# Optimization experiments

Hardware: AMD Instinct MI355X
Metric: run time of the kernel (lower is better)

The kernel has to match this reference:

```python
import jax, jax.numpy as jnp
import numpy as np

N, E = 10000, 160000          # nodes, edges
MUL = 128                     # channel multiplicity of 0e and 1o blocks
NSP = 10                      # node_attrs (species one-hot) dim
NRAD = 8                      # edge_feats radial basis dim
SILU_C = 1.6790               # e3nn normalize2mom constant for SiLU
AVG_NEIGH = 16.0
SQ3 = np.sqrt(3.0).astype(np.float32)


def setup_inputs() -> dict:
    key = jax.random.key(0)
    ks = jax.random.split(key, 14)
    d = {}
    d["node_feats"] = jax.random.normal(ks[0], (N, 4 * MUL), jnp.float32)   # [N, 128 + 128*3]
    d["node_attrs"] = jax.random.normal(ks[1], (N, NSP), jnp.float32)
    d["edge_feats"] = jax.random.normal(ks[2], (E, NRAD), jnp.float32)
    d["edge_attrs"] = jax.random.normal(ks[3], (E, 4), jnp.float32)          # [0e | 1o]
    d["edge_index"] = jax.random.randint(ks[4], (2, E), 0, N, jnp.int32)
    # e3nn internal weights are standard normal; normalization applied in forward
    d["lin1_ws"] = jax.random.normal(ks[5], (MUL, MUL), jnp.float32)
    d["lin1_wv"] = jax.random.normal(ks[6], (MUL, MUL), jnp.float32)
    d["fc_w0"] = jax.random.normal(ks[7], (NRAD, 64), jnp.float32)
    d["fc_w1"] = jax.random.normal(ks[8], (64, 64), jnp.float32)
    d["fc_w2"] = jax.random.normal(ks[9], (64, 4 * MUL), jnp.float32)        # tp.weight_numel = 512
    d["lin2_ws"] = jax.random.normal(ks[10], (2 * MUL, MUL), jnp.float32)    # 256x0e -> 128x0e
    d["lin2_wv"] = jax.random.normal(ks[11], (2 * MUL, MUL), jnp.float32)    # 256x1o -> 128x1o
    d["sc_ws"] = jax.random.normal(ks[12], (MUL, NSP, MUL), jnp.float32)
    d["sc_wv"] = jax.random.normal(ks[13], (MUL, NSP, MUL), jnp.float32)
    return d


def _fc(ef, w0, w1, w2):
    # e3nn FullyConnectedNet: x @ W / sqrt(fan_in), normalize2mom-scaled SiLU between layers
    h = SILU_C * jax.nn.silu(ef @ w0 / np.float32(np.sqrt(NRAD)))
    h = SILU_C * jax.nn.silu(h @ w1 / np.float32(8.0))
    return h @ w2 / np.float32(8.0)


def reference(node_feats, node_attrs, edge_feats, edge_attrs, edge_index,
              lin1_ws, lin1_wv, fc_w0, fc_w1, fc_w2,
              lin2_ws, lin2_wv, sc_ws, sc_wv):
    x_s = node_feats[:, :MUL]                       # [N, 128] scalar block
    x_v = node_feats[:, MUL:].reshape(N, MUL, 3)    # [N, 128, 3] vector block

    # self-connection: FullyConnectedTensorProduct with 10x0e attrs; path weight 1/sqrt(mul1*mul2)
    sc_norm = np.float32(1.0 / np.sqrt(MUL * NSP))
    sc_s = jnp.einsum('nu,nv,uvw->nw', x_s, node_attrs, sc_ws) * sc_norm
    sc_v = jnp.einsum('nuc,nv,uvw->nwc', x_v, node_attrs, sc_wv) * sc_norm

    # linear_1 (per-irrep channel mixing, fan_in = 128)
    l1 = np.float32(1.0 / np.sqrt(MUL))
    y_s = (x_s @ lin1_ws) * l1
    y_v = jnp.einsum('nuc,uw->nwc', x_v, lin1_wv) * l1

    src = edge_index[1]
    dst = edge_index[0]
    xs_e = y_s[src]                                 # [E, 128]
    xv_e = y_v[src]                                 # [E, 128, 3]
    a_s = edge_attrs[:, :1]                         # [E, 1]
    a_v = edge_attrs[:, 1:]                         # [E, 3]

    w = _fc(edge_feats, fc_w0, fc_w1, fc_w2)        # [E, 512]
    w_ss, w_sv, w_vs, w_vv = jnp.split(w, 4, axis=1)  # instruction order in source

    # 'uvu' weighted tensor product with e3nn component/element normalization:
    # net coefficient per path works out to 1 except 1o x 1o -> 0e which is 1/sqrt(3)
    mid_s0 = w_ss * xs_e * a_s                                          # 0e*0e->0e
    mid_s1 = w_vv * jnp.einsum('euc,ec->eu', xv_e, a_v) / SQ3           # 1o*1o->0e
    mid_v2 = (w_sv * xs_e)[:, :, None] * a_v[:, None, :]                # 0e*1o->1o
    mid_v3 = w_vs[:, :, None] * xv_e * a_s[:, :, None]                  # 1o*0e->1o

    inv = np.float32(1.0 / np.sqrt(AVG_NEIGH))
    s = jax.ops.segment_sum(jnp.concatenate([mid_s0, mid_s1], axis=1), dst, num_segments=N) * inv  # [N, 256]
    v = jax.ops.segment_sum(jnp.concatenate([mid_v2, mid_v3], axis=1), dst, num_segments=N) * inv  # [N, 256, 3]

    # linear_2 (fan_in = 256)
    l2 = np.float32(1.0 / np.sqrt(2 * MUL))
    out_s = (s @ lin2_ws) * l2 + sc_s
    out_v = jnp.einsum('nuc,uw->nwc', v, lin2_wv) * l2 + sc_v

    return jnp.concatenate([out_s, out_v.reshape(N, 3 * MUL)], axis=1)   # [N, 512]
```

## Files before the change

### kernel.cpp

```cpp
#include <hip/hip_runtime.h>
#include <hip/hip_bf16.h>
#include <math.h>

#define N_NODES 10000
#define N_EDGES 160000
#define SO_BLK 157
#define VO_BLK 469

typedef __attribute__((ext_vector_type(8))) short short8x;
typedef __attribute__((ext_vector_type(4))) float floatx4;
typedef __attribute__((ext_vector_type(4))) unsigned int uint4x;
typedef __attribute__((ext_vector_type(2))) unsigned int uint2x;

union S8 { short8x v; unsigned short u[8]; uint4 q; };
union U2 { uint2x v; unsigned short us[4]; };

__device__ __forceinline__ unsigned short f2bf(float x) {
    unsigned int u = __float_as_uint(x);
    return (unsigned short)((u + 0x7fffu + ((u >> 16) & 1u)) >> 16);
}
__device__ __forceinline__ float bf2f(unsigned short u) {
    return __uint_as_float(((unsigned)u) << 16);
}
__device__ __forceinline__ float silu_c(float x) {
    return 1.679f * x / (1.0f + __expf(-x));
}

__global__ __launch_bounds__(256) void pack_all_kernel(
    const float* __restrict__ sc_ws, const float* __restrict__ lin2_ws,
    const float* __restrict__ sc_wv, const float* __restrict__ lin2_wv,
    const float* __restrict__ fc_w2, const float* __restrict__ fc_w1,
    const float* __restrict__ lin1_ws, const float* __restrict__ lin1_wv,
    unsigned short* __restrict__ b_pre, unsigned short* __restrict__ w2a,
    unsigned short* __restrict__ w1a, unsigned short* __restrict__ b_lin)
{
    const int bid = blockIdx.x;
    const int t = threadIdx.x;
    if (bid < 192) {
        int id = bid * 256 + t;
        int mat = id / 24576;
        int slot = id - mat * 24576;
        int ks = slot >> 9;
        int rr = slot & 511;
        int lane = rr & 63;
        int quad = lane >> 4;
        int n = ((rr >> 6) << 4) + (lane & 15);
        const float* sc  = mat ? sc_wv  : sc_ws;
        const float* lin = mat ? lin2_wv : lin2_ws;
        S8 pk;
        #pragma unroll
        for (int j = 0; j < 8; j++) {
            int k = ks * 32 + quad * 8 + j;
            float w;
            if (k < 1280) {
                int u = k & 127, v = k >> 7;
                w = sc[(u * 10 + v) * 128 + n];
            } else {
                w = lin[(k - 1280) * 128 + n];
            }
            pk.u[j] = f2bf(w);
        }
        *(uint4*)(b_pre + (size_t)id * 8) = pk.q;
    } else if (bid < 208) {
        int id = (bid - 192) * 256 + t;
        int lane = id & 63;
        int mfg = (id >> 6) & 31;
        int ks = id >> 11;
        int col = mfg * 16 + (lane & 15);
        int k0 = ks * 32 + (lane >> 4) * 8;
        S8 pk;
        #pragma unroll
        for (int j = 0; j < 8; j++)
            pk.u[j] = f2bf(fc_w2[(k0 + j) * 512 + col] * 0.125f);
        *(uint4*)(w2a + (size_t)id * 8) = pk.q;
    } else if (bid < 210) {
        int id = (bid - 208) * 256 + t;
        int lane = id & 63;
        int mf = (id >> 6) & 3;
        int ks = id >> 8;
        int m = mf * 16 + (lane & 15);
        int k0 = ks * 32 + (lane >> 4) * 8;
        S8 pk;
        #pragma unroll
        for (int j = 0; j < 8; j++)
            pk.u[j] = f2bf(fc_w1[(k0 + j) * 64 + m] * 0.125f);
        *(uint4*)(w1a + (size_t)id * 8) = pk.q;
    } else {
        int id = (bid - 210) * 256 + t;
        int mat = id >> 11;
        int slot = id & 2047;
        int ks = slot >> 9;
        int rr = slot & 511;
        int nf = rr >> 6;
        int lane = rr & 63;
        int n = nf * 16 + (lane & 15);
        int k0 = ks * 32 + (lane >> 4) * 8;
        const float* w = mat ? lin1_wv : lin1_ws;
        const float l1 = 0.0883883476483f;
        S8 pk;
        #pragma unroll
        for (int j = 0; j < 8; j++)
            pk.u[j] = f2bf(w[(k0 + j) * 128 + n] * l1);
        *(uint4*)(b_lin + (size_t)id * 8) = pk.q;
    }
}

__global__ __launch_bounds__(256) void node_lin1_mfma(
    const float* __restrict__ node_feats,
    const unsigned short* __restrict__ b_lin,
    unsigned short* __restrict__ y_pk,
    unsigned short* __restrict__ xvP16)
{
    __shared__ __align__(16) unsigned char smem[32768];
    short8x* Al = (short8x*)smem;
    unsigned short* Yt = (unsigned short*)smem;

    const int blk = blockIdx.x;
    const int t = threadIdx.x;
    const int base = blk * 32;
    const int lane = t & 63;
    const int wv = t >> 6;
    const int m15 = lane & 15;
    const int k0q = (lane >> 4) * 8;

    #pragma unroll
    for (int it = 0; it < 8; it++) {
        int g = wv * 8 + it;
        int af = g >> 2;
        int ks = g & 3;
        int m = af * 16 + m15;
        int comp = m >> 5;
        int nloc = m & 31;
        int node = base + nloc;
        int valid = (node < N_NODES);
        if (!valid) node = N_NODES - 1;
        int k0 = ks * 32 + k0q;
        const float* row = node_feats + (size_t)node * 512;
        S8 pk;
        if (comp == 0) {
            float4 a = *(const float4*)&row[k0];
            float4 b = *(const float4*)&row[k0 + 4];
            pk.u[0] = f2bf(a.x); pk.u[1] = f2bf(a.y); pk.u[2] = f2bf(a.z); pk.u[3] = f2bf(a.w);
            pk.u[4] = f2bf(b.x); pk.u[5] = f2bf(b.y); pk.u[6] = f2bf(b.z); pk.u[7] = f2bf(b.w);
        } else {
            int c = comp - 1;
            #pragma unroll
            for (int j = 0; j < 8; j++)
                pk.u[j] = f2bf(row[128 + (k0 + j) * 3 + c]);
            if (valid)
                *(uint4*)&xvP16[((size_t)node * 3 + c) * 128 + k0] = pk.q;
        }
        Al[(ks * 8 + af) * 64 + lane] = pk.v;
    }
    __syncthreads();

    floatx4 c[8][2];
    #pragma unroll
    for (int af = 0; af < 8; af++) {
        c[af][0] = (floatx4){0.f, 0.f, 0.f, 0.f};
        c[af][1] = (floatx4){0.f, 0.f, 0.f, 0.f};
    }

    const uint4* bq = (const uint4*)b_lin;
    #pragma unroll
    for (int ks = 0; ks < 4; ks++) {
        S8 bs0, bs1, bv0, bv1;
        bs0.q = bq[       ks*512 + (wv*2+0)*64 + lane];
        bs1.q = bq[       ks*512 + (wv*2+1)*64 + lane];
        bv0.q = bq[2048 + ks*512 + (wv*2+0)*64 + lane];
        bv1.q = bq[2048 + ks*512 + (wv*2+1)*64 + lane];
        #pragma unroll
        for (int af = 0; af < 8; af++) {
            short8x a = Al[(ks*8 + af)*64 + lane];
            if (af < 2) {
                c[af][0] = __builtin_amdgcn_mfma_f32_16x16x32_bf16(a, bs0.v, c[af][0], 0, 0, 0);
                c[af][1] = __builtin_amdgcn_mfma_f32_16x16x32_bf16(a, bs1.v, c[af][1], 0, 0, 0);
            } else {
                c[af][0] = __builtin_amdgcn_mfma_f32_16x16x32_bf16(a, bv0.v, c[af][0], 0, 0, 0);
                c[af][1] = __builtin_amdgcn_mfma_f32_16x16x32_bf16(a, bv1.v, c[af][1], 0, 0, 0);
            }
        }
    }
    __syncthreads();

    {
        const int rq = (lane >> 4) * 4;
        #pragma unroll
        for (int af = 0; af < 8; af++) {
            #pragma unroll
            for (int nf = 0; nf < 2; nf++) {
                int u = wv * 32 + nf * 16 + m15;
                #pragma unroll
                for (int i = 0; i < 4; i++) {
                    int m = af * 16 + rq + i;
                    int comp = m >> 5, nloc = m & 31;
                    Yt[(nloc * 128 + u) * 4 + comp] = f2bf(c[af][nf][i]);
                }
            }
        }
    }
    __syncthreads();
    {
        unsigned short* dst = y_pk + (size_t)base * 512;
        int nrem = N_NODES - base;
        #pragma unroll
        for (int it = 0; it < 8; it++) {
            int idx = it * 256 + t;
            if ((idx >> 6) < nrem)
                *(uint4*)(dst + (size_t)idx * 8) = *(const uint4*)&Yt[idx * 8];
        }
    }
}

__global__ __launch_bounds__(256) void hist_kernel(const int* __restrict__ edge_index,
                                                   int* __restrict__ deg) {
    int e = blockIdx.x * 256 + threadIdx.x;
    if (e < N_EDGES) atomicAdd(&deg[edge_index[e]], 1);
}

__global__ __launch_bounds__(1024) void scan_kernel(const int* __restrict__ deg,
                                                    int* __restrict__ row_start,
                                                    int* __restrict__ cursor) {
    __shared__ int wsum[16];
    __shared__ int carry_s;
    const int t = threadIdx.x;
    const int lane = t & 63, w = t >> 6;
    if (t == 0) carry_s = 0;
    __syncthreads();
    for (int chunk = 0; chunk < 10; chunk++) {
        int idx = chunk * 1024 + t;
        int v = (idx < N_NODES) ? deg[idx] : 0;
        int x = v;
        #pragma unroll
        for (int off = 1; off < 64; off <<= 1) {
            int yv = __shfl_up(x, off, 64);
            if (lane >= off) x += yv;
        }
        if (lane == 63) wsum[w] = x;
        __syncthreads();
        int wpre = 0;
        for (int i = 0; i < w; i++) wpre += wsum[i];
        int incl = x + wpre + carry_s;
        int excl = incl - v;
        if (idx < N_NODES) { row_start[idx] = excl; cursor[idx] = excl; }
        __syncthreads();
        if (t == 1023) carry_s = incl;
        __syncthreads();
    }
    if (t == 0) row_start[N_NODES] = carry_s;
}

__global__ __launch_bounds__(256) void scatter_kernel(const int* __restrict__ edge_index,
                                                      const float* __restrict__ edge_attrs,
                                                      int* __restrict__ cursor,
                                                      int* __restrict__ edge_list,
                                                      int* __restrict__ srcs,
                                                      float* __restrict__ ea_sorted) {
    int e = blockIdx.x * 256 + threadIdx.x;
    if (e < N_EDGES) {
        int pos = atomicAdd(&cursor[edge_index[e]], 1);
        edge_list[pos] = e;
        srcs[pos] = edge_index[N_EDGES + e];
        float4 ea = *(const float4*)(edge_attrs + (size_t)e * 4);
        *(float4*)(ea_sorted + (size_t)pos * 4) = ea;
    }
}

__global__ __launch_bounds__(256) void edge_w_mfma(
    const float* __restrict__ edge_feats,
    const int* __restrict__ edge_list,
    const float* __restrict__ fc_w0,
    const unsigned short* __restrict__ w1a,
    const unsigned short* __restrict__ w2a,
    unsigned short* __restrict__ w_pk)
{
    __shared__ __align__(16) unsigned char smem[26368];
    float* ef = (float*)smem;
    unsigned short* h0b = (unsigned short*)(smem + 2304);
    unsigned short* T   = (unsigned short*)smem;
    unsigned short* h1b = (unsigned short*)(smem + 16896);
    int* eids = (int*)(smem + 26112);

    const int blk = blockIdx.x;
    const int t = threadIdx.x;
    const int eb0 = blk * 64;
    const int lane = t & 63;
    const int wv = t >> 6;
    const int quad = lane >> 4;
    const int m15 = lane & 15;

    if (t < 64) eids[t] = edge_list[eb0 + t];
    __syncthreads();

    #pragma unroll
    for (int r = 0; r < 2; r++) {
        int idx = r * 256 + t;
        int el = idx >> 3;
        int k = idx & 7;
        ef[el * 9 + k] = edge_feats[(size_t)eids[el] * 8 + k];
    }
    __syncthreads();

    {
        const int e_loc = t >> 2;
        const int c0 = (t & 3) * 16;
        float a0[16];
        #pragma unroll
        for (int i = 0; i < 16; i++) a0[i] = 0.f;
        const float* efr = &ef[e_loc * 9];
        #pragma unroll
        for (int k = 0; k < 8; k++) {
            float ek = efr[k];
            float w[16];
            #pragma unroll
            for (int q4 = 0; q4 < 4; q4++)
                *(float4*)&w[q4*4] = *(const float4*)&fc_w0[k*64 + c0 + q4*4];
            #pragma unroll
            for (int i = 0; i < 16; i++) a0[i] += ek * w[i];
        }
        const float is8 = 0.35355339059f;
        S8 p0, p1;
        #pragma unroll
        for (int i = 0; i < 8; i++) {
            p0.u[i] = f2bf(silu_c(a0[i] * is8));
            p1.u[i] = f2bf(silu_c(a0[8 + i] * is8));
        }
        *(uint4*)&h0b[e_loc * 72 + c0]     = p0.q;
        *(uint4*)&h0b[e_loc * 72 + c0 + 8] = p1.q;
    }
    __syncthreads();

    {
        floatx4 c2[4];
        #pragma unroll
        for (int ee = 0; ee < 4; ee++) c2[ee] = (floatx4){0.f, 0.f, 0.f, 0.f};
        const uint4* w1aq = (const uint4*)w1a;
        #pragma unroll
        for (int ks = 0; ks < 2; ks++) {
            S8 afr;
            afr.q = w1aq[(ks*4 + wv)*64 + lane];
            #pragma unroll
            for (int ee = 0; ee < 4; ee++) {
                S8 bfr;
                bfr.q = *(const uint4*)&h0b[(ee*16 + m15) * 72 + ks*32 + quad*8];
                c2[ee] = __builtin_amdgcn_mfma_f32_16x16x32_bf16(afr.v, bfr.v, c2[ee], 0, 0, 0);
            }
        }
        #pragma unroll
        for (int ee = 0; ee < 4; ee++) {
            ushort4 pk = make_ushort4(f2bf(silu_c(c2[ee][0])), f2bf(silu_c(c2[ee][1])),
                                      f2bf(silu_c(c2[ee][2])), f2bf(silu_c(c2[ee][3])));
            *(ushort4*)&h1b[(ee*16 + m15) * 72 + wv*16 + quad*4] = pk;
        }
    }
    __syncthreads();

    const uint4* w2aq = (const uint4*)w2a;
    #pragma unroll 1
    for (int p = 0; p < 4; p++) {
        floatx4 c3[2][4];
        #pragma unroll
        for (int mf = 0; mf < 2; mf++)
            #pragma unroll
            for (int ee = 0; ee < 4; ee++)
                c3[mf][ee] = (floatx4){0.f, 0.f, 0.f, 0.f};

        #pragma unroll
        for (int ks = 0; ks < 2; ks++) {
            S8 bfr[4];
            #pragma unroll
            for (int ee = 0; ee < 4; ee++)
                bfr[ee].q = *(const uint4*)&h1b[(ee*16 + m15) * 72 + ks*32 + quad*8];
            #pragma unroll
            for (int mf = 0; mf < 2; mf++) {
                S8 afr;
                afr.q = w2aq[(size_t)(ks*32 + wv*8 + p*2 + mf) * 64 + lane];
                #pragma unroll
                for (int ee = 0; ee < 4; ee++)
                    c3[mf][ee] = __builtin_amdgcn_mfma_f32_16x16x32_bf16(afr.v, bfr[ee].v, c3[mf][ee], 0, 0, 0);
            }
        }

        __syncthreads();
        #pragma unroll
        for (int mf = 0; mf < 2; mf++) {
            #pragma unroll
            for (int ee = 0; ee < 4; ee++) {
                int e = ee*16 + m15;
                #pragma unroll
                for (int i = 0; i < 4; i++) {
                    int colp = mf*16 + quad*4 + i;
                    T[e*132 + colp*4 + wv] = f2bf(c3[mf][ee][i]);
                }
            }
        }
        __syncthreads();

        #pragma unroll
        for (int it = 0; it < 8; it++) {
            int idx = it * 256 + t;
            int e  = idx >> 5;
            int cu = idx & 31;
            uint2x v = *(const uint2x*)&T[e*132 + cu*4];
            unsigned short* dstp = w_pk + ((size_t)(eb0 + e) * 128 + p*32 + cu) * 4;
            __builtin_nontemporal_store(v, (uint2x*)dstp);
        }
    }
}

__global__ __launch_bounds__(256) void gather_kernel(
    const int* __restrict__ row_start,
    const int* __restrict__ srcs,
    const float* __restrict__ ea_sorted,
    const unsigned short* __restrict__ w_pk,
    const unsigned short* __restrict__ y_pk,
    float* __restrict__ accS,
    float* __restrict__ accV)
{
    __shared__ float sm[2][128][9];
    const int t = threadIdx.x;
    const int h = t >> 7;
    const int u = t & 127;
    const int n = blockIdx.x;
    const int sbeg = row_start[n];
    const int send = row_start[n + 1];

    float aS0 = 0.f, aS1 = 0.f;
    float aV2x = 0.f, aV2y = 0.f, aV2z = 0.f;
    float aV3x = 0.f, aV3y = 0.f, aV3z = 0.f;

    if (sbeg < send) {
        const int last = send - 1;
        const int i0 = sbeg + h;

        int j0 = (i0     < send) ? i0     : last;
        int j1 = (i0 + 2 < send) ? i0 + 2 : last;
        int s0 = srcs[j0];
        int s1 = srcs[j1];

        U2 wqA, wqB; ushort4 yqA, yqB; float4 eaA, eaB;
        wqA.v = __builtin_nontemporal_load((const uint2x*)(w_pk + ((size_t)j0 * 128 + u) * 4));
        eaA   = *(const float4*)(ea_sorted + (size_t)j0 * 4);
        yqA   = *(const ushort4*)(y_pk + ((size_t)s0 * 128 + u) * 4);
        wqB.v = __builtin_nontemporal_load((const uint2x*)(w_pk + ((size_t)j1 * 128 + u) * 4));
        eaB   = *(const float4*)(ea_sorted + (size_t)j1 * 4);
        yqB   = *(const ushort4*)(y_pk + ((size_t)s1 * 128 + u) * 4);

        int sP0 = srcs[(i0 + 4 < send) ? i0 + 4 : last];
        int sP1 = srcs[(i0 + 6 < send) ? i0 + 6 : last];

        for (int i = i0; i < send; i += 4) {
            {
                float wss = bf2f(wqA.us[0]), wsv = bf2f(wqA.us[1]);
                float wvs = bf2f(wqA.us[2]), wvv = bf2f(wqA.us[3]);
                float qs = bf2f(yqA.x), q0 = bf2f(yqA.y), q1 = bf2f(yqA.z), q2 = bf2f(yqA.w);
                aS0 += wss * qs * eaA.x;
                aS1 += wvv * (q0*eaA.y + q1*eaA.z + q2*eaA.w);
                float tsv = wsv * qs;
                aV2x += tsv * eaA.y; aV2y += tsv * eaA.z; aV2z += tsv * eaA.w;
                float tvs = wvs * eaA.x;
                aV3x += tvs * q0; aV3y += tvs * q1; aV3z += tvs * q2;
            }
            {
                int jn = (i + 4 < send) ? i + 4 : last;
                wqA.v = __builtin_nontemporal_load((const uint2x*)(w_pk + ((size_t)jn * 128 + u) * 4));
                eaA   = *(const float4*)(ea_sorted + (size_t)jn * 4);
                yqA   = *(const ushort4*)(y_pk + ((size_t)sP0 * 128 + u) * 4);
                sP0 = srcs[(i + 8 < send) ? i + 8 : last];
            }
            {
                float m = (i + 2 < send) ? 1.f : 0.f;
                float ex = eaB.x * m, ey = eaB.y * m, ez = eaB.z * m, ew = eaB.w * m;
                float wss = bf2f(wqB.us[0]), wsv = bf2f(wqB.us[1]);
                float wvs = bf2f(wqB.us[2]), wvv = bf2f(wqB.us[3]);
                float qs = bf2f(yqB.x), q0 = bf2f(yqB.y), q1 = bf2f(yqB.z), q2 = bf2f(yqB.w);
                aS0 += wss * qs * ex;
                aS1 += wvv * (q0*ey + q1*ez + q2*ew);
                float tsv = wsv * qs;
                aV2x += tsv * ey; aV2y += tsv * ez; aV2z += tsv * ew;
                float tvs = wvs * ex;
                aV3x += tvs * q0; aV3y += tvs * q1; aV3z += tvs * q2;
            }
            {
                int jn = (i + 6 < send) ? i + 6 : last;
                wqB.v = __builtin_nontemporal_load((const uint2x*)(w_pk + ((size_t)jn * 128 + u) * 4));
                eaB   = *(const float4*)(ea_sorted + (size_t)jn * 4);
                yqB   = *(const ushort4*)(y_pk + ((size_t)sP1 * 128 + u) * 4);
                sP1 = srcs[(i + 10 < send) ? i + 10 : last];
            }
        }
    }

    sm[h][u][0] = aS0;  sm[h][u][1] = aS1;
    sm[h][u][2] = aV2x; sm[h][u][3] = aV2y;
    sm[h][u][4] = aV2z; sm[h][u][5] = aV3x;
    sm[h][u][6] = aV3y; sm[h][u][7] = aV3z;
    __syncthreads();

    const float inv = 0.25f;
    const float s1c = 0.57735026919f * 0.25f;
    if (h == 0) {
        float v0 = sm[0][u][0] + sm[1][u][0];
        float v1 = sm[0][u][1] + sm[1][u][1];
        float v2 = sm[0][u][2] + sm[1][u][2];
        float v3 = sm[0][u][3] + sm[1][u][3];
        accS[(size_t)n * 256 + u]       = v0 * inv;
        accS[(size_t)n * 256 + 128 + u] = v1 * s1c;
        accV[((size_t)n * 3 + 0) * 256 + u] = v2 * inv;
        accV[((size_t)n * 3 + 1) * 256 + u] = v3 * inv;
    } else {
        float v4 = sm[0][u][4] + sm[1][u][4];
        float v5 = sm[0][u][5] + sm[1][u][5];
        float v6 = sm[0][u][6] + sm[1][u][6];
        float v7 = sm[0][u][7] + sm[1][u][7];
        accV[((size_t)n * 3 + 2) * 256 + u]       = v4 * inv;
        accV[((size_t)n * 3 + 0) * 256 + 128 + u] = v5 * inv;
        accV[((size_t)n * 3 + 1) * 256 + 128 + u] = v6 * inv;
        accV[((size_t)n * 3 + 2) * 256 + 128 + u] = v7 * inv;
    }
}

__global__ __launch_bounds__(256) void node_out_mfma(
    const float* __restrict__ node_feats,
    const float* __restrict__ node_attrs,
    const unsigned short* __restrict__ xvP16,
    const float* __restrict__ accS,
    const float* __restrict__ accV,
    const unsigned short* __restrict__ b_pre,
    float* __restrict__ out)
{
    __shared__ __align__(16) short8x Abuf[2][256];
    const int bid = blockIdx.x;
    const int t = threadIdx.x;
    const int lane = t & 63;
    const int wv = t >> 6;
    const bool is_s = (bid < SO_BLK);

    const int r    = ((t >> 6) << 4) + (t & 15);
    const int q8   = ((t >> 4) & 3) * 8;

    const float* px = nullptr;
    const unsigned short* pxv = nullptr;
    const float* pa;
    const float* pat;
    if (is_s) {
        int R = bid * 64 + r;
        int node = (R < N_NODES) ? R : 0;
        px  = node_feats + (size_t)node * 512;
        pa  = accS + (size_t)node * 256;
        pat = node_attrs + node * 10;
    } else {
        int Rg = (bid - SO_BLK) * 64 + r;
        if (Rg >= 3 * N_NODES) Rg = 0;
        int node = Rg / 3;
        pxv = xvP16 + (size_t)Rg * 128;
        pa  = accV + (size_t)Rg * 256;
        pat = node_attrs + node * 10;
    }

    const uint4* bb = (const uint4*)(b_pre) + (is_s ? 0 : 24576);
    const float sc_norm = 0.02795084972f;
    const float l2 = 0.0625f;

    float xf[4][8];
    S8    xh[4];
    if (is_s) {
        #pragma unroll
        for (int c = 0; c < 4; c++) {
            floatx4 lo = *(const floatx4*)&px[c*32 + q8];
            floatx4 hi = *(const floatx4*)&px[c*32 + q8 + 4];
            #pragma unroll
            for (int i = 0; i < 4; i++) { xf[c][i] = lo[i]; xf[c][4+i] = hi[i]; }
        }
    } else {
        #pragma unroll
        for (int c = 0; c < 4; c++)
            xh[c].q = *(const uint4*)&pxv[c*32 + q8];
    }
    float attC = pat[0] * sc_norm;

    floatx4 acc[4][2];
    #pragma unroll
    for (int af = 0; af < 4; af++) {
        acc[af][0] = (floatx4){0.f, 0.f, 0.f, 0.f};
        acc[af][1] = (floatx4){0.f, 0.f, 0.f, 0.f};
    }

    const int cof0 = (wv*2+0)*64 + lane;
    const int cof1 = (wv*2+1)*64 + lane;

    auto packx = [&](int c_, float att_) -> short8x {
        S8 pk;
        if (is_s) {
            #pragma unroll
            for (int i = 0; i < 8; i++) pk.u[i] = f2bf(xf[c_][i] * att_);
        } else {
            #pragma unroll
            for (int i = 0; i < 8; i++) pk.u[i] = f2bf(bf2f(xh[c_].u[i]) * att_);
        }
        return pk.v;
    };
    auto mstep = [&](int kb, const S8& b0, const S8& b1) {
        __builtin_amdgcn_s_setprio(1);
        #pragma unroll
        for (int af = 0; af < 4; af++) {
            short8x a = Abuf[kb][af*64 + lane];
            acc[af][0] = __builtin_amdgcn_mfma_f32_16x16x32_bf16(a, b0.v, acc[af][0], 0, 0, 0);
            acc[af][1] = __builtin_amdgcn_mfma_f32_16x16x32_bf16(a, b1.v, acc[af][1], 0, 0, 0);
        }
        __builtin_amdgcn_s_setprio(0);
    };
    auto bload = [&](int k2, S8& b0, S8& b1) {
        b0.q = bb[(size_t)k2*512 + cof0];
        b1.q = bb[(size_t)k2*512 + cof1];
    };
    auto barrier_ = [&]() {
        asm volatile("s_waitcnt lgkmcnt(0)" ::: "memory");
        __builtin_amdgcn_s_barrier();
    };

    S8 bA0, bA1, bB0, bB1;
    bload(0, bA0, bA1);
    bload(1, bB0, bB1);

    Abuf[0][t] = packx(0, attC);
    barrier_();

    #pragma unroll 1
    for (int vb = 0; vb < 9; vb++) {
        float attN = pat[vb + 1] * sc_norm;
        const int ksb = vb * 4;
        Abuf[1][t] = packx(1, attC); mstep(0, bA0, bA1); bload(ksb+2, bA0, bA1); barrier_();
        Abuf[0][t] = packx(2, attC); mstep(1, bB0, bB1); bload(ksb+3, bB0, bB1); barrier_();
        Abuf[1][t] = packx(3, attC); mstep(0, bA0, bA1); bload(ksb+4, bA0, bA1); barrier_();
        Abuf[0][t] = packx(0, attN); mstep(1, bB0, bB1); bload(ksb+5, bB0, bB1); barrier_();
        attC = attN;
    }

    floatx4 aT0[2], aT1[2];
    auto issue0 = [&](int k_) { int j2 = (k_-40)*32 + q8;
        aT0[0] = *(const floatx4*)&pa[j2]; aT0[1] = *(const floatx4*)&pa[j2+4]; };
    auto issue1 = [&](int k_) { int j2 = (k_-40)*32 + q8;
        aT1[0] = *(const floatx4*)&pa[j2]; aT1[1] = *(const floatx4*)&pa[j2+4]; };
    auto packT = [&](const floatx4* a2) -> short8x {
        S8 pk;
        #pragma unroll
        for (int i = 0; i < 4; i++) { pk.u[i] = f2bf(a2[0][i] * l2); pk.u[4+i] = f2bf(a2[1][i] * l2); }
        return pk.v;
    };

    Abuf[1][t] = packx(1, attC); mstep(0, bA0, bA1); bload(38, bA0, bA1); barrier_();
    Abuf[0][t] = packx(2, attC); mstep(1, bB0, bB1); bload(39, bB0, bB1); barrier_();
    issue0(40);
    Abuf[1][t] = packx(3, attC); mstep(0, bA0, bA1); bload(40, bA0, bA1); barrier_();
    issue1(41);
    Abuf[0][t] = packT(aT0); mstep(1, bB0, bB1); bload(41, bB0, bB1); barrier_();
    issue0(42);
    Abuf[1][t] = packT(aT1); mstep(0, bA0, bA1); bload(42, bA0, bA1); barrier_();
    issue1(43);
    Abuf[0][t] = packT(aT0); mstep(1, bB0, bB1); bload(43, bB0, bB1); barrier_();
    issue0(44);
    Abuf[1][t] = packT(aT1); mstep(0, bA0, bA1); bload(44, bA0, bA1); barrier_();
    issue1(45);
    Abuf[0][t] = packT(aT0); mstep(1, bB0, bB1); bload(45, bB0, bB1); barrier_();
    issue0(46);
    Abuf[1][t] = packT(aT1); mstep(0, bA0, bA1); bload(46, bA0, bA1); barrier_();
    issue1(47);
    Abuf[0][t] = packT(aT0); mstep(1, bB0, bB1); bload(47, bB0, bB1); barrier_();
    Abuf[1][t] = packT(aT1); mstep(0, bA0, bA1); barrier_();
    mstep(1, bB0, bB1);

    const int m = lane & 15;
    const int rq = (lane >> 4) * 4;
    if (is_s) {
        const int n0 = bid * 64;
        #pragma unroll
        for (int af = 0; af < 4; af++) {
            #pragma unroll
            for (int i = 0; i < 4; i++) {
                int n = n0 + af*16 + rq + i;
                if (n < N_NODES) {
                    out[(size_t)n*512 + wv*32 + m]      = acc[af][0][i];
                    out[(size_t)n*512 + wv*32 + 16 + m] = acc[af][1][i];
                }
            }
        }
    } else {
        const int r0 = (bid - SO_BLK) * 64;
        #pragma unroll
        for (int af = 0; af < 4; af++) {
            #pragma unroll
            for (int i = 0; i < 4; i++) {
                int Rg = r0 + af*16 + rq + i;
                if (Rg < 3 * N_NODES) {
                    int nn = Rg / 3;
                    int cc = Rg - nn * 3;
                    float* po = out + (size_t)nn*512 + 128 + cc;
                    po[(wv*32 + m)*3]      = acc[af][0][i];
                    po[(wv*32 + 16 + m)*3] = acc[af][1][i];
                }
            }
        }
    }
}

extern "C" void kernel_launch(void* const* d_in, const int* in_sizes, int n_in,
                              void* d_out, int out_size, void* d_ws, size_t ws_size,
                              hipStream_t stream) {
    const float* node_feats = (const float*)d_in[0];
    const float* node_attrs = (const float*)d_in[1];
    const float* edge_feats = (const float*)d_in[2];
    const float* edge_attrs = (const float*)d_in[3];
    const int*   edge_index = (const int*)  d_in[4];
    const float* lin1_ws    = (const float*)d_in[5];
    const float* lin1_wv    = (const float*)d_in[6];
    const float* fc_w0      = (const float*)d_in[7];
    const float* fc_w1      = (const float*)d_in[8];
    const float* fc_w2      = (const float*)d_in[9];
    const float* lin2_ws    = (const float*)d_in[10];
    const float* lin2_wv    = (const float*)d_in[11];
    const float* sc_ws      = (const float*)d_in[12];
    const float* sc_wv      = (const float*)d_in[13];
    float* out = (float*)d_out;

    unsigned short* y_pk  = (unsigned short*)d_ws;
    float* accS = (float*)(y_pk + (size_t)5120000);
    float* accV = accS + (size_t)2560000;
    unsigned short* xvP16 = (unsigned short*)(accV + (size_t)7680000);
    unsigned short* w_pk  = xvP16 + (size_t)3840000;
    int* deg       = (int*)(w_pk + (size_t)81920000);
    int* row_start = deg + 10016;
    int* cursor    = row_start + 10016;
    int* edge_list = cursor + 10016;
    int* srcs      = edge_list + N_EDGES;
    float* ea_sorted = (float*)(srcs + N_EDGES);
    unsigned short* b_pre = (unsigned short*)(ea_sorted + (size_t)N_EDGES * 4);
    unsigned short* w2a   = b_pre + (size_t)2 * 24576 * 8;
    unsigned short* w1a   = w2a + (size_t)4096 * 8;
    unsigned short* b_lin = w1a + (size_t)512 * 8;
    const size_t need = (size_t)5120000 * 2 + (size_t)(2560000 + 7680000) * 4
                      + (size_t)3840000 * 2 + (size_t)81920000 * 2
                      + (size_t)(10016 * 3 + N_EDGES * 2) * 4
                      + (size_t)N_EDGES * 4 * 4
                      + ((size_t)2 * 24576 * 8 + (size_t)4096 * 8 + (size_t)512 * 8
                         + (size_t)4096 * 8) * 2;
    if (ws_size < need) return;

    hipLaunchKernelGGL(pack_all_kernel, dim3(226), dim3(256), 0, stream,
                       sc_ws, lin2_ws, sc_wv, lin2_wv, fc_w2, fc_w1, lin1_ws, lin1_wv,
                       b_pre, w2a, w1a, b_lin);
    hipLaunchKernelGGL(node_lin1_mfma, dim3(313), dim3(256), 0, stream,
                       node_feats, b_lin, y_pk, xvP16);

    hipMemsetAsync(deg, 0, (size_t)N_NODES * sizeof(int), stream);
    hipLaunchKernelGGL(hist_kernel, dim3(625), dim3(256), 0, stream, edge_index, deg);
    hipLaunchKernelGGL(scan_kernel, dim3(1), dim3(1024), 0, stream, deg, row_start, cursor);
    hipLaunchKernelGGL(scatter_kernel, dim3(625), dim3(256), 0, stream,
                       edge_index, edge_attrs, cursor, edge_list, srcs, ea_sorted);
    hipLaunchKernelGGL(edge_w_mfma, dim3(2500), dim3(256), 0, stream,
                       edge_feats, edge_list, fc_w0, w1a, w2a, w_pk);
    hipLaunchKernelGGL(gather_kernel, dim3(N_NODES), dim3(256), 0, stream,
                       row_start, srcs, ea_sorted, w_pk, y_pk, accS, accV);

    hipLaunchKernelGGL(node_out_mfma, dim3(SO_BLK + VO_BLK), dim3(256), 0, stream,
                       node_feats, node_attrs, xvP16, accS, accV, b_pre, out);
}
```

Before: 289.5 us.

## Assign two nodes per wavefront in gather with per-edge destination tracking

The gather kernel now gives each wavefront two consecutive nodes instead of one 256-thread block per node. Each lane handles two channels with 128-bit loads and walks the merged edge range, using a new sorted destination array to flush accumulators at node boundaries. This drops the shared-memory reduction and __syncthreads, cuts the grid from 10000 blocks to 1250, and widens the loads. In exchange the scatter kernel writes an extra dsts array, and nodes with uneven degree can unbalance work across wavefronts.

```diff
diff --git a/kernel.cpp b/kernel.cpp
--- a/kernel.cpp
+++ b/kernel.cpp
@@ -12,7 +12,7 @@
 typedef __attribute__((ext_vector_type(4))) unsigned int uint4x;
 typedef __attribute__((ext_vector_type(2))) unsigned int uint2x;
 
-union S8 { short8x v; unsigned short u[8]; uint4 q; };
+union S8 { short8x v; unsigned short u[8]; uint4 q; uint4x qx; };
 union U2 { uint2x v; unsigned short us[4]; };
 
 __device__ __forceinline__ unsigned short f2bf(float x) {
@@ -255,12 +255,15 @@
                                                       int* __restrict__ cursor,
                                                       int* __restrict__ edge_list,
                                                       int* __restrict__ srcs,
+                                                      int* __restrict__ dsts,
                                                       float* __restrict__ ea_sorted) {
     int e = blockIdx.x * 256 + threadIdx.x;
     if (e < N_EDGES) {
-        int pos = atomicAdd(&cursor[edge_index[e]], 1);
+        int dd = edge_index[e];
+        int pos = atomicAdd(&cursor[dd], 1);
         edge_list[pos] = e;
         srcs[pos] = edge_index[N_EDGES + e];
+        dsts[pos] = dd;
         float4 ea = *(const float4*)(edge_attrs + (size_t)e * 4);
         *(float4*)(ea_sorted + (size_t)pos * 4) = ea;
     }
@@ -411,113 +414,116 @@
 __global__ __launch_bounds__(256) void gather_kernel(
     const int* __restrict__ row_start,
     const int* __restrict__ srcs,
+    const int* __restrict__ dsts,
     const float* __restrict__ ea_sorted,
     const unsigned short* __restrict__ w_pk,
     const unsigned short* __restrict__ y_pk,
     float* __restrict__ accS,
     float* __restrict__ accV)
 {
-    __shared__ float sm[2][128][9];
     const int t = threadIdx.x;
-    const int h = t >> 7;
-    const int u = t & 127;
-    const int n = blockIdx.x;
-    const int sbeg = row_start[n];
-    const int send = row_start[n + 1];
-
-    float aS0 = 0.f, aS1 = 0.f;
-    float aV2x = 0.f, aV2y = 0.f, aV2z = 0.f;
-    float aV3x = 0.f, aV3y = 0.f, aV3z = 0.f;
-
-    if (sbeg < send) {
-        const int last = send - 1;
-        const int i0 = sbeg + h;
-
-        int j0 = (i0     < send) ? i0     : last;
-        int j1 = (i0 + 2 < send) ? i0 + 2 : last;
-        int s0 = srcs[j0];
-        int s1 = srcs[j1];
-
-        U2 wqA, wqB; ushort4 yqA, yqB; float4 eaA, eaB;
-        wqA.v = __builtin_nontemporal_load((const uint2x*)(w_pk + ((size_t)j0 * 128 + u) * 4));
-        eaA   = *(const float4*)(ea_sorted + (size_t)j0 * 4);
-        yqA   = *(const ushort4*)(y_pk + ((size_t)s0 * 128 + u) * 4);
-        wqB.v = __builtin_nontemporal_load((const uint2x*)(w_pk + ((size_t)j1 * 128 + u) * 4));
-        eaB   = *(const float4*)(ea_sorted + (size_t)j1 * 4);
-        yqB   = *(const ushort4*)(y_pk + ((size_t)s1 * 128 + u) * 4);
-
-        int sP0 = srcs[(i0 + 4 < send) ? i0 + 4 : last];
-        int sP1 = srcs[(i0 + 6 < send) ? i0 + 6 : last];
-
-        for (int i = i0; i < send; i += 4) {
-            {
-                float wss = bf2f(wqA.us[0]), wsv = bf2f(wqA.us[1]);
-                float wvs = bf2f(wqA.us[2]), wvv = bf2f(wqA.us[3]);
-                float qs = bf2f(yqA.x), q0 = bf2f(yqA.y), q1 = bf2f(yqA.z), q2 = bf2f(yqA.w);
-                aS0 += wss * qs * eaA.x;
-                aS1 += wvv * (q0*eaA.y + q1*eaA.z + q2*eaA.w);
-                float tsv = wsv * qs;
-                aV2x += tsv * eaA.y; aV2y += tsv * eaA.z; aV2z += tsv * eaA.w;
-                float tvs = wvs * eaA.x;
-                aV3x += tvs * q0; aV3y += tvs * q1; aV3z += tvs * q2;
-            }
-            {
-                int jn = (i + 4 < send) ? i + 4 : last;
-                wqA.v = __builtin_nontemporal_load((const uint2x*)(w_pk + ((size_t)jn * 128 + u) * 4));
-                eaA   = *(const float4*)(ea_sorted + (size_t)jn * 4);
-                yqA   = *(const ushort4*)(y_pk + ((size_t)sP0 * 128 + u) * 4);
-                sP0 = srcs[(i + 8 < send) ? i + 8 : last];
-            }
-            {
-                float m = (i + 2 < send) ? 1.f : 0.f;
-                float ex = eaB.x * m, ey = eaB.y * m, ez = eaB.z * m, ew = eaB.w * m;
-                float wss = bf2f(wqB.us[0]), wsv = bf2f(wqB.us[1]);
-                float wvs = bf2f(wqB.us[2]), wvv = bf2f(wqB.us[3]);
-                float qs = bf2f(yqB.x), q0 = bf2f(yqB.y), q1 = bf2f(yqB.z), q2 = bf2f(yqB.w);
-                aS0 += wss * qs * ex;
-                aS1 += wvv * (q0*ey + q1*ez + q2*ew);
-                float tsv = wsv * qs;
-                aV2x += tsv * ey; aV2y += tsv * ez; aV2z += tsv * ew;
-                float tvs = wvs * ex;
-                aV3x += tvs * q0; aV3y += tvs * q1; aV3z += tvs * q2;
-            }
-            {
-                int jn = (i + 6 < send) ? i + 6 : last;
-                wqB.v = __builtin_nontemporal_load((const uint2x*)(w_pk + ((size_t)jn * 128 + u) * 4));
-                eaB   = *(const float4*)(ea_sorted + (size_t)jn * 4);
-                yqB   = *(const ushort4*)(y_pk + ((size_t)sP1 * 128 + u) * 4);
-                sP1 = srcs[(i + 10 < send) ? i + 10 : last];
-            }
-        }
-    }
-
-    sm[h][u][0] = aS0;  sm[h][u][1] = aS1;
-    sm[h][u][2] = aV2x; sm[h][u][3] = aV2y;
-    sm[h][u][4] = aV2z; sm[h][u][5] = aV3x;
-    sm[h][u][6] = aV3y; sm[h][u][7] = aV3z;
-    __syncthreads();
+    const int wv = t >> 6;
+    const int lane = t & 63;
+    const int u0 = lane << 1;
+    int cur = blockIdx.x * 8 + wv * 2;
+    const int nb_end = cur + 2;
+
+    const int eb = row_start[cur];
+    const int ee = row_start[nb_end];
+
+    float aS0a=0.f,aS0b=0.f, aS1a=0.f,aS1b=0.f;
+    float aV2ax=0.f,aV2ay=0.f,aV2az=0.f, aV2bx=0.f,aV2by=0.f,aV2bz=0.f;
+    float aV3ax=0.f,aV3ay=0.f,aV3az=0.f, aV3bx=0.f,aV3by=0.f,aV3bz=0.f;
 
     const float inv = 0.25f;
     const float s1c = 0.57735026919f * 0.25f;
-    if (h == 0) {
-        float v0 = sm[0][u][0] + sm[1][u][0];
-        float v1 = sm[0][u][1] + sm[1][u][1];
-        float v2 = sm[0][u][2] + sm[1][u][2];
-        float v3 = sm[0][u][3] + sm[1][u][3];
-        accS[(size_t)n * 256 + u]       = v0 * inv;
-        accS[(size_t)n * 256 + 128 + u] = v1 * s1c;
-        accV[((size_t)n * 3 + 0) * 256 + u] = v2 * inv;
-        accV[((size_t)n * 3 + 1) * 256 + u] = v3 * inv;
-    } else {
-        float v4 = sm[0][u][4] + sm[1][u][4];
-        float v5 = sm[0][u][5] + sm[1][u][5];
-        float v6 = sm[0][u][6] + sm[1][u][6];
-        float v7 = sm[0][u][7] + sm[1][u][7];
-        accV[((size_t)n * 3 + 2) * 256 + u]       = v4 * inv;
-        accV[((size_t)n * 3 + 0) * 256 + 128 + u] = v5 * inv;
-        accV[((size_t)n * 3 + 1) * 256 + 128 + u] = v6 * inv;
-        accV[((size_t)n * 3 + 2) * 256 + 128 + u] = v7 * inv;
-    }
+
+    auto flush = [&](int n) {
+        *(float2*)(accS + (size_t)n*256 + u0)        = make_float2(aS0a*inv, aS0b*inv);
+        *(float2*)(accS + (size_t)n*256 + 128 + u0)  = make_float2(aS1a*s1c, aS1b*s1c);
+        *(float2*)(accV + ((size_t)n*3+0)*256 + u0)       = make_float2(aV2ax*inv, aV2bx*inv);
+        *(float2*)(accV + ((size_t)n*3+0)*256 + 128 + u0) = make_float2(aV3ax*inv, aV3bx*inv);
+        *(float2*)(accV + ((size_t)n*3+1)*256 + u0)       = make_float2(aV2ay*inv, aV2by*inv);
+        *(float2*)(accV + ((size_t)n*3+1)*256 + 128 + u0) = make_float2(aV3ay*inv, aV3by*inv);
+        *(float2*)(accV + ((size_t)n*3+2)*256 + u0)       = make_float2(aV2az*inv, aV2bz*inv);
+        *(float2*)(accV + ((size_t)n*3+2)*256 + 128 + u0) = make_float2(aV3az*inv, aV3bz*inv);
+        aS0a=aS0b=aS1a=aS1b=0.f;
+        aV2ax=aV2ay=aV2az=aV2bx=aV2by=aV2bz=0.f;
+        aV3ax=aV3ay=aV3az=aV3bx=aV3by=aV3bz=0.f;
+    };
+
+    auto consume = [&](const S8& w8, const S8& y8, const float4& ea) {
+        {
+            float wss = bf2f(w8.u[0]), wsv = bf2f(w8.u[1]);
+            float wvs = bf2f(w8.u[2]), wvv = bf2f(w8.u[3]);
+            float qs = bf2f(y8.u[0]), q0 = bf2f(y8.u[1]), q1 = bf2f(y8.u[2]), q2 = bf2f(y8.u[3]);
+            aS0a += wss * qs * ea.x;
+            aS1a += wvv * (q0*ea.y + q1*ea.z + q2*ea.w);
+            float tsv = wsv * qs;
+            aV2ax += tsv * ea.y; aV2ay += tsv * ea.z; aV2az += tsv * ea.w;
+            float tvs = wvs * ea.x;
+            aV3ax += tvs * q0; aV3ay += tvs * q1; aV3az += tvs * q2;
+        }
+        {
+            float wss = bf2f(w8.u[4]), wsv = bf2f(w8.u[5]);
+            float wvs = bf2f(w8.u[6]), wvv = bf2f(w8.u[7]);
+            float qs = bf2f(y8.u[4]), q0 = bf2f(y8.u[5]), q1 = bf2f(y8.u[6]), q2 = bf2f(y8.u[7]);
+            aS0b += wss * qs * ea.x;
+            aS1b += wvv * (q0*ea.y + q1*ea.z + q2*ea.w);
+            float tsv = wsv * qs;
+            aV2bx += tsv * ea.y; aV2by += tsv * ea.z; aV2bz += tsv * ea.w;
+            float tvs = wvs * ea.x;
+            aV3bx += tvs * q0; aV3by += tvs * q1; aV3bz += tvs * q2;
+        }
+    };
+
+    if (eb < ee) {
+        const int last = N_EDGES - 1;
+        int jB0 = (eb+1 < last) ? eb+1 : last;
+        int j2  = (eb+2 < last) ? eb+2 : last;
+        int j3  = (eb+3 < last) ? eb+3 : last;
+
+        int sA = srcs[eb],  dA = dsts[eb];
+        int sB = srcs[jB0], dB = dsts[jB0];
+        int sP0 = srcs[j2], dP0 = dsts[j2];
+        int sP1 = srcs[j3], dP1 = dsts[j3];
+
+        S8 wA, wB, yA, yB; float4 eaA, eaB;
+        wA.qx = __builtin_nontemporal_load((const uint4x*)(w_pk + ((size_t)eb * 128 + u0) * 4));
+        eaA  = *(const float4*)(ea_sorted + (size_t)eb * 4);
+        yA.q = *(const uint4*)(y_pk + ((size_t)sA * 128 + u0) * 4);
+        wB.qx = __builtin_nontemporal_load((const uint4x*)(w_pk + ((size_t)jB0 * 128 + u0) * 4));
+        eaB  = *(const float4*)(ea_sorted + (size_t)jB0 * 4);
+        yB.q = *(const uint4*)(y_pk + ((size_t)sB * 128 + u0) * 4);
+
+        for (int i = eb; i < ee; i += 2) {
+            while (cur < dA) flush(cur++);
+            consume(wA, yA, eaA);
+            {
+                int jn = (i+2 < last) ? i+2 : last;
+                wA.qx = __builtin_nontemporal_load((const uint4x*)(w_pk + ((size_t)jn * 128 + u0) * 4));
+                eaA  = *(const float4*)(ea_sorted + (size_t)jn * 4);
+                yA.q = *(const uint4*)(y_pk + ((size_t)sP0 * 128 + u0) * 4);
+                dA = dP0;
+                int j4 = (i+4 < last) ? i+4 : last;
+                sP0 = srcs[j4]; dP0 = dsts[j4];
+            }
+            if (i + 1 < ee) {
+                while (cur < dB) flush(cur++);
+                consume(wB, yB, eaB);
+            }
+            {
+                int jn = (i+3 < last) ? i+3 : last;
+                wB.qx = __builtin_nontemporal_load((const uint4x*)(w_pk + ((size_t)jn * 128 + u0) * 4));
+                eaB  = *(const float4*)(ea_sorted + (size_t)jn * 4);
+                yB.q = *(const uint4*)(y_pk + ((size_t)sP1 * 128 + u0) * 4);
+                dB = dP1;
+                int j5 = (i+5 < last) ? i+5 : last;
+                sP1 = srcs[j5]; dP1 = dsts[j5];
+            }
+        }
+    }
+    while (cur < nb_end) flush(cur++);
 }
 
 __global__ __launch_bounds__(256) void node_out_mfma(
@@ -733,14 +739,15 @@
     int* cursor    = row_start + 10016;
     int* edge_list = cursor + 10016;
     int* srcs      = edge_list + N_EDGES;
-    float* ea_sorted = (float*)(srcs + N_EDGES);
+    int* dsts      = srcs + N_EDGES;
+    float* ea_sorted = (float*)(dsts + N_EDGES);
     unsigned short* b_pre = (unsigned short*)(ea_sorted + (size_t)N_EDGES * 4);
     unsigned short* w2a   = b_pre + (size_t)2 * 24576 * 8;
     unsigned short* w1a   = w2a + (size_t)4096 * 8;
     unsigned short* b_lin = w1a + (size_t)512 * 8;
     const size_t need = (size_t)5120000 * 2 + (size_t)(2560000 + 7680000) * 4
                       + (size_t)3840000 * 2 + (size_t)81920000 * 2
-                      + (size_t)(10016 * 3 + N_EDGES * 2) * 4
+                      + (size_t)(10016 * 3 + N_EDGES * 3) * 4
                       + (size_t)N_EDGES * 4 * 4
                       + ((size_t)2 * 24576 * 8 + (size_t)4096 * 8 + (size_t)512 * 8
                          + (size_t)4096 * 8) * 2;
@@ -756,11 +763,11 @@
     hipLaunchKernelGGL(hist_kernel, dim3(625), dim3(256), 0, stream, edge_index, deg);
     hipLaunchKernelGGL(scan_kernel, dim3(1), dim3(1024), 0, stream, deg, row_start, cursor);
     hipLaunchKernelGGL(scatter_kernel, dim3(625), dim3(256), 0, stream,
-                       edge_index, edge_attrs, cursor, edge_list, srcs, ea_sorted);
+                       edge_index, edge_attrs, cursor, edge_list, srcs, dsts, ea_sorted);
     hipLaunchKernelGGL(edge_w_mfma, dim3(2500), dim3(256), 0, stream,
                        edge_feats, edge_list, fc_w0, w1a, w2a, w_pk);
-    hipLaunchKernelGGL(gather_kernel, dim3(N_NODES), dim3(256), 0, stream,
-                       row_start, srcs, ea_sorted, w_pk, y_pk, accS, accV);
+    hipLaunchKernelGGL(gather_kernel, dim3(1250), dim3(256), 0, stream,
+                       row_start, srcs, dsts, ea_sorted, w_pk, y_pk, accS, accV);
 
     hipLaunchKernelGGL(node_out_mfma, dim3(SO_BLK + VO_BLK), dim3(256), 0, stream,
                        node_feats, node_attrs, xvP16, accS, accV, b_pre, out);
```

Result: no change. 289.8 us (+0.1%).
